# Kernel optimization log

Measured on AMD Instinct MI355X. Metric: run time of the kernel, lower is better.

## Reference

```python
import jax, jax.numpy as jnp
import numpy as np

IN_FEATURES = 1024
OUT_FEATURES = 1024
GRID_SIZE = 8
SPLINE_ORDER = 3
NUM_CTRL = GRID_SIZE + SPLINE_ORDER  # 11


def _make_grid():
    h = 2.0 / GRID_SIZE
    return jnp.linspace(-1.0 - SPLINE_ORDER * h, 1.0 + SPLINE_ORDER * h,
                        GRID_SIZE + 2 * SPLINE_ORDER + 1, dtype=jnp.float32)  # [15]


def b_splines(t, grid, order):
    # t: [B, F] (already tanh'd). Vectorized over all features at once —
    # the torch per-feature Python loop computes identical math per column.
    te = t[..., None]  # [B, F, 1]
    basis = ((te >= grid[:-1]) & (te < grid[1:])).astype(t.dtype)  # [B, F, G-1]
    for k in range(1, order + 1):
        left_den = grid[k:-1] - grid[:-k - 1]
        left_den = jnp.where(left_den == 0, jnp.ones_like(left_den), left_den)
        left = (te - grid[:-k - 1]) / left_den * basis[..., :-1]
        right_den = grid[k + 1:] - grid[1:-k]
        right_den = jnp.where(right_den == 0, jnp.ones_like(right_den), right_den)
        right = (grid[k + 1:] - te) / right_den * basis[..., 1:]
        basis = left + right
    return basis  # [B, F, NUM_CTRL]


def setup_inputs() -> dict:
    key = jax.random.key(0)
    kx, kc, kw = jax.random.split(key, 3)
    x = jax.random.normal(kx, (4096, IN_FEATURES), dtype=jnp.float32)
    coeffs = jax.random.normal(kc, (IN_FEATURES, OUT_FEATURES, NUM_CTRL), dtype=jnp.float32) * 0.05
    base_weight = jax.random.normal(kw, (IN_FEATURES, OUT_FEATURES), dtype=jnp.float32) * 0.05
    grid = _make_grid()
    return {"x": x, "coeffs": coeffs, "base_weight": base_weight, "grid": grid}


def reference(x, coeffs, base_weight, grid):
    bases = b_splines(jnp.tanh(x), grid, SPLINE_ORDER)          # [B, in, n]
    activation = jnp.einsum('bin,ion->bo', bases, coeffs)        # [B, out]
    residual = x @ base_weight                                   # [B, out]
    return activation + residual
```

## Files before the change

### kernel.cpp

```cpp
#include <hip/hip_runtime.h>
#include <hip/hip_bf16.h>

typedef __attribute__((ext_vector_type(8))) short bf16x8;
typedef __attribute__((ext_vector_type(4))) float f32x4;
typedef __attribute__((ext_vector_type(4))) unsigned short u16x4;
typedef __attribute__((ext_vector_type(8))) unsigned short u16x8;

#define M_DIM 4096
#define N_DIM 1024
#define IN_F  1024
#define K_DIM 12288
#define KS2   2
#define KPART2 (K_DIM / KS2)
#define BK 64
#define NT (KPART2 / BK)

__device__ __forceinline__ unsigned short f2b(float v) {
  __hip_bfloat16 h = __float2bfloat16(v);
  return *reinterpret_cast<unsigned short*>(&h);
}

__device__ __forceinline__ void spline12(float xv, float* w) {
  float t  = tanhf(xv);
  float tf = (t + 1.75f) * 4.0f;
  int j = (int)tf;
  j = j < 3 ? 3 : (j > 10 ? 10 : j);
  float u  = tf - (float)j;
  float um = 1.0f - u;
  float u2 = u * u;
  float w0 = um * um * um * (1.0f / 6.0f);
  float w1 = (0.5f * u - 1.0f) * u2 + (2.0f / 3.0f);
  float w2 = ((-0.5f * u + 0.5f) * u + 0.5f) * u + (1.0f / 6.0f);
  float w3 = u * u2 * (1.0f / 6.0f);
  int base = j - 3;
  #pragma unroll
  for (int s = 0; s < 11; ++s) {
    int r = s - base;
    w[s] = (r == 0) ? w0 : (r == 1) ? w1 : (r == 2) ? w2 : (r == 3) ? w3 : 0.0f;
  }
  w[11] = xv;
}

__global__ __launch_bounds__(256) void bases_kernel(const float* __restrict__ x,
                                                    unsigned short* __restrict__ A) {
  int e0 = blockIdx.x * 512 + threadIdx.x * 2;
  float2 xv = *(const float2*)(x + e0);
  float w0[12], w1[12];
  spline12(xv.x, w0);
  spline12(xv.y, w1);
  unsigned short h[24];
  #pragma unroll
  for (int s = 0; s < 12; ++s) { h[s] = f2b(w0[s]); h[12 + s] = f2b(w1[s]); }
  u16x8* dst = (u16x8*)(A + (size_t)e0 * 12);
  dst[0] = (u16x8){h[0],  h[1],  h[2],  h[3],  h[4],  h[5],  h[6],  h[7]};
  dst[1] = (u16x8){h[8],  h[9],  h[10], h[11], h[12], h[13], h[14], h[15]};
  dst[2] = (u16x8){h[16], h[17], h[18], h[19], h[20], h[21], h[22], h[23]};
}

__global__ __launch_bounds__(256) void repack_kernel(const float* __restrict__ coeffs,
                                                     const float* __restrict__ W,
                                                     unsigned short* __restrict__ Bt) {
  __shared__ float lc[64 * 176];
  __shared__ float lw[64 * 16];
  const int o0 = blockIdx.x * 16;
  const int i0 = blockIdx.y * 64;
  const int tid = threadIdx.x;
  #pragma unroll
  for (int it = 0; it < 11; ++it) {
    int v = it * 256 + tid;
    int i = v / 44, c = v - i * 44;
    f32x4 d = *(const f32x4*)(coeffs + ((size_t)(i0 + i) * 1024 + o0) * 11 + c * 4);
    *(f32x4*)(lc + i * 176 + c * 4) = d;
  }
  #pragma unroll
  for (int it = 0; it < 4; ++it) {
    int e = it * 256 + tid;
    int i = e >> 4, ol = e & 15;
    lw[e] = W[(size_t)(i0 + i) * 1024 + o0 + ol];
  }
  __syncthreads();
  #pragma unroll
  for (int it = 0; it < 6; ++it) {
    int v = it * 256 + tid;
    int ol = v / 96, c = v - ol * 96;
    unsigned short h[8];
    #pragma unroll
    for (int s = 0; s < 8; ++s) {
      int g = c * 8 + s;
      int i = g / 12, n = g - i * 12;
      float val = (n < 11) ? lc[i * 176 + ol * 11 + n] : lw[i * 16 + ol];
      h[s] = f2b(val);
    }
    *(u16x8*)(Bt + (size_t)(o0 + ol) * K_DIM + (size_t)i0 * 12 + c * 8) =
        (u16x8){h[0], h[1], h[2], h[3], h[4], h[5], h[6], h[7]};
  }
}

__device__ __forceinline__ void async16(const void* g, void* l) {
  __builtin_amdgcn_global_load_lds(
      (const __attribute__((address_space(1))) void*)g,
      (__attribute__((address_space(3))) void*)l, 16, 0, 0);
}

__global__ __launch_bounds__(512, 1) void gemm_kernel(const unsigned short* __restrict__ A,
                                                      const unsigned short* __restrict__ Bt,
                                                      float* __restrict__ out) {
  __shared__ __align__(16) unsigned short lds[73728];
  char* lp = (char*)lds;
  const int AS0 = 0, AS1 = 32768, AS2 = 65536;
  const int BS0 = 98304, BS1 = 98304 + 16384, BS2 = 98304 + 32768;

  const int tid  = threadIdx.x;
  const int lane = tid & 63;
  const int wid  = tid >> 6;
  const int wm   = wid >> 1;
  const int wn   = wid & 1;

  const int blk = blockIdx.x;
  const int bn  = blk & 7;
  const int r   = blk >> 3;
  const int bm  = r & 15;
  const int ks  = r >> 4;
  const size_t m0 = (size_t)bm * 256;
  const size_t n0 = (size_t)bn * 128;
  const size_t ksbyte = (size_t)ks * KPART2 * 2;

  const char* srcA[4]; int ldsA[4];
  #pragma unroll
  for (int q = 0; q < 4; ++q) {
    int g = q * 512 + tid;
    int rr = g >> 3, cp = g & 7;
    int cs = cp ^ (rr & 7);
    srcA[q] = (const char*)A + ((m0 + rr) * (size_t)K_DIM) * 2 + ksbyte + cs * 16;
    ldsA[q] = g * 16;
  }
  const char* srcB[2]; int ldsB[2];
  #pragma unroll
  for (int q = 0; q < 2; ++q) {
    int g = q * 512 + tid;
    int rr = g >> 3, cp = g & 7;
    int cs = cp ^ (rr & 7);
    srcB[q] = (const char*)Bt + ((n0 + rr) * (size_t)K_DIM) * 2 + ksbyte + cs * 16;
    ldsB[q] = g * 16;
  }

  auto stage = [&](int sa, int sb, int tile) {
    size_t kb = (size_t)tile * 128;
    #pragma unroll
    for (int q = 0; q < 4; ++q) async16(srcA[q] + kb, lp + sa + ldsA[q]);
    #pragma unroll
    for (int q = 0; q < 2; ++q) async16(srcB[q] + kb, lp + sb + ldsB[q]);
  };

  int offA[2][4], offB[2][4];
  #pragma unroll
  for (int kk = 0; kk < 2; ++kk) {
    #pragma unroll
    for (int m = 0; m < 4; ++m) {
      int row = wm * 64 + m * 16 + (lane & 15);
      int ck  = (kk * 4 + (lane >> 4)) ^ (row & 7);
      offA[kk][m] = row * 128 + ck * 16;
    }
    #pragma unroll
    for (int n = 0; n < 4; ++n) {
      int rowb = wn * 64 + n * 16 + (lane & 15);
      int ckb  = (kk * 4 + (lane >> 4)) ^ (rowb & 7);
      offB[kk][n] = rowb * 128 + ckb * 16;
    }
  }

  f32x4 acc[4][4];
  #pragma unroll
  for (int m = 0; m < 4; ++m)
    #pragma unroll
    for (int n = 0; n < 4; ++n) acc[m][n] = (f32x4){0.f, 0.f, 0.f, 0.f};

  stage(AS0, BS0, 0);
  stage(AS1, BS1, 1);
  stage(AS2, BS2, 2);

  int cA = AS0, nA = AS1, fA = AS2;
  int cB = BS0, nB = BS1, fB = BS2;

  for (int t = 0; t < NT; ++t) {
    if (t < NT - 2)       asm volatile("s_waitcnt vmcnt(12)" ::: "memory");
    else if (t == NT - 2) asm volatile("s_waitcnt vmcnt(6)"  ::: "memory");
    else                  asm volatile("s_waitcnt vmcnt(0)"  ::: "memory");
    __builtin_amdgcn_s_barrier();
    __builtin_amdgcn_sched_barrier(0);
    asm volatile("" ::: "memory");

    __builtin_amdgcn_s_setprio(1);
    #pragma unroll
    for (int kk = 0; kk < 2; ++kk) {
      bf16x8 a[4], b[4];
      #pragma unroll
      for (int m = 0; m < 4; ++m) a[m] = *(const bf16x8*)(lp + cA + offA[kk][m]);
      #pragma unroll
      for (int n = 0; n < 4; ++n) b[n] = *(const bf16x8*)(lp + cB + offB[kk][n]);
      #pragma unroll
      for (int m = 0; m < 4; ++m)
        #pragma unroll
        for (int n = 0; n < 4; ++n)
          acc[m][n] = __builtin_amdgcn_mfma_f32_16x16x32_bf16(a[m], b[n], acc[m][n], 0, 0, 0);
    }
    __builtin_amdgcn_s_setprio(0);

    asm volatile("" ::: "memory");
    __builtin_amdgcn_sched_barrier(0);
    __builtin_amdgcn_s_barrier();

    if (t + 3 < NT) stage(cA, cB, t + 3);

    int ta = cA; cA = nA; nA = fA; fA = ta;
    int tb = cB; cB = nB; nB = fB; fB = tb;
  }

  const int lr = (lane >> 4) * 4;
  const int lc = lane & 15;
  #pragma unroll
  for (int m = 0; m < 4; ++m)
    #pragma unroll
    for (int n = 0; n < 4; ++n)
      #pragma unroll
      for (int j = 0; j < 4; ++j)
        atomicAdd(&out[(m0 + wm * 64 + m * 16 + lr + j) * N_DIM + n0 + wn * 64 + n * 16 + lc],
                  acc[m][n][j]);
}

__global__ __launch_bounds__(256) void fallback_kernel(const float* __restrict__ x,
                                                       const float* __restrict__ coeffs,
                                                       const float* __restrict__ W,
                                                       float* __restrict__ out) {
  __shared__ float bas[16][64][12];
  const int o0 = blockIdx.x * 64;
  const int b0 = blockIdx.y * 16;
  const int tid = threadIdx.x;
  const int o = tid & 63, bg = tid >> 6;
  float acc[4] = {0.f, 0.f, 0.f, 0.f};
  for (int ic = 0; ic < 16; ++ic) {
    __syncthreads();
    #pragma unroll
    for (int p = 0; p < 4; ++p) {
      int pp = tid + p * 256;
      int bb = pp >> 6, il = pp & 63;
      float w[12];
      spline12(x[(size_t)(b0 + bb) * 1024 + ic * 64 + il], w);
      #pragma unroll
      for (int n = 0; n < 12; ++n) bas[bb][il][n] = w[n];
    }
    __syncthreads();
    for (int il = 0; il < 64; ++il) {
      int gi = ic * 64 + il;
      const float* cp = coeffs + ((size_t)gi * 1024 + o0 + o) * 11;
      float cf[12];
      #pragma unroll
      for (int n = 0; n < 11; ++n) cf[n] = cp[n];
      cf[11] = W[(size_t)gi * 1024 + o0 + o];
      #pragma unroll
      for (int bb = 0; bb < 4; ++bb) {
        float s = 0.f;
        #pragma unroll
        for (int n = 0; n < 12; ++n) s += bas[bg * 4 + bb][il][n] * cf[n];
        acc[bb] += s;
      }
    }
  }
  #pragma unroll
  for (int bb = 0; bb < 4; ++bb)
    out[(size_t)(b0 + bg * 4 + bb) * 1024 + o0 + o] = acc[bb];
}

extern "C" void kernel_launch(void* const* d_in, const int* in_sizes, int n_in,
                              void* d_out, int out_size, void* d_ws, size_t ws_size,
                              hipStream_t stream) {
  const float* x      = (const float*)d_in[0];
  const float* coeffs = (const float*)d_in[1];
  const float* W      = (const float*)d_in[2];
  float* out = (float*)d_out;

  const size_t needA = (size_t)M_DIM * K_DIM * 2;
  const size_t needB = (size_t)N_DIM * K_DIM * 2;

  if (ws_size >= needA + needB) {
    unsigned short* Abuf = (unsigned short*)d_ws;
    unsigned short* Btuf = (unsigned short*)((char*)d_ws + needA);
    hipMemsetAsync(out, 0, (size_t)out_size * sizeof(float), stream);
    bases_kernel<<<dim3(M_DIM * IN_F / 512), dim3(256), 0, stream>>>(x, Abuf);
    repack_kernel<<<dim3(64, 16), dim3(256), 0, stream>>>(coeffs, W, Btuf);
    gemm_kernel<<<dim3(16 * 8 * KS2), dim3(512), 0, stream>>>(Abuf, Btuf, out);
  } else {
    fallback_kernel<<<dim3(16, 256), dim3(256), 0, stream>>>(x, coeffs, W, out);
  }
}
```

Baseline: 276.7 us.

## Shrink GEMM tiles to 128x128 with double buffering and XCD-aware block mapping

The GEMM moves from 256x128 tiles with 512 threads and triple buffering to 128x128 tiles with 256 threads, double buffering and two blocks per CU. The grid grows to 512 blocks, and blocks are mapped so each XCD handles a contiguous set of M rows, which should help L2 reuse and occupancy. The bases kernel now stages its output through shared memory so global stores are coalesced, and repack LDS strides are padded to reduce bank conflicts. Smaller tiles reuse each loaded byte less, and two-stage buffering hides less latency than three.

New measurement: 236.9 us. 1.17x faster.

```diff
diff --git a/kernel.cpp b/kernel.cpp
--- a/kernel.cpp
+++ b/kernel.cpp
@@ -3,7 +3,6 @@
 
 typedef __attribute__((ext_vector_type(8))) short bf16x8;
 typedef __attribute__((ext_vector_type(4))) float f32x4;
-typedef __attribute__((ext_vector_type(4))) unsigned short u16x4;
 typedef __attribute__((ext_vector_type(8))) unsigned short u16x8;
 
 #define M_DIM 4096
@@ -11,9 +10,9 @@
 #define IN_F  1024
 #define K_DIM 12288
 #define KS2   2
-#define KPART2 (K_DIM / KS2)
+#define KPART (K_DIM / KS2)
 #define BK 64
-#define NT (KPART2 / BK)
+#define NT (KPART / BK)
 
 __device__ __forceinline__ unsigned short f2b(float v) {
   __hip_bfloat16 h = __float2bfloat16(v);
@@ -43,25 +42,27 @@
 
 __global__ __launch_bounds__(256) void bases_kernel(const float* __restrict__ x,
                                                     unsigned short* __restrict__ A) {
-  int e0 = blockIdx.x * 512 + threadIdx.x * 2;
+  __shared__ unsigned short sb[256 * 24];
+  const int tid = threadIdx.x;
+  int e0 = blockIdx.x * 512 + tid * 2;
   float2 xv = *(const float2*)(x + e0);
   float w0[12], w1[12];
   spline12(xv.x, w0);
   spline12(xv.y, w1);
-  unsigned short h[24];
-  #pragma unroll
-  for (int s = 0; s < 12; ++s) { h[s] = f2b(w0[s]); h[12 + s] = f2b(w1[s]); }
-  u16x8* dst = (u16x8*)(A + (size_t)e0 * 12);
-  dst[0] = (u16x8){h[0],  h[1],  h[2],  h[3],  h[4],  h[5],  h[6],  h[7]};
-  dst[1] = (u16x8){h[8],  h[9],  h[10], h[11], h[12], h[13], h[14], h[15]};
-  dst[2] = (u16x8){h[16], h[17], h[18], h[19], h[20], h[21], h[22], h[23]};
+  #pragma unroll
+  for (int s = 0; s < 12; ++s) { sb[tid * 24 + s] = f2b(w0[s]); sb[tid * 24 + 12 + s] = f2b(w1[s]); }
+  __syncthreads();
+  u16x8* dst = (u16x8*)(A + (size_t)blockIdx.x * 512 * 12);
+  const u16x8* src = (const u16x8*)sb;
+  #pragma unroll
+  for (int k = 0; k < 3; ++k) dst[tid + k * 256] = src[tid + k * 256];
 }
 
 __global__ __launch_bounds__(256) void repack_kernel(const float* __restrict__ coeffs,
                                                      const float* __restrict__ W,
                                                      unsigned short* __restrict__ Bt) {
-  __shared__ float lc[64 * 176];
-  __shared__ float lw[64 * 16];
+  __shared__ float lc[64 * 180];
+  __shared__ float lw[64 * 20];
   const int o0 = blockIdx.x * 16;
   const int i0 = blockIdx.y * 64;
   const int tid = threadIdx.x;
@@ -70,13 +71,13 @@
     int v = it * 256 + tid;
     int i = v / 44, c = v - i * 44;
     f32x4 d = *(const f32x4*)(coeffs + ((size_t)(i0 + i) * 1024 + o0) * 11 + c * 4);
-    *(f32x4*)(lc + i * 176 + c * 4) = d;
+    *(f32x4*)(lc + i * 180 + c * 4) = d;
   }
   #pragma unroll
   for (int it = 0; it < 4; ++it) {
     int e = it * 256 + tid;
     int i = e >> 4, ol = e & 15;
-    lw[e] = W[(size_t)(i0 + i) * 1024 + o0 + ol];
+    lw[i * 20 + ol] = W[(size_t)(i0 + i) * 1024 + o0 + ol];
   }
   __syncthreads();
   #pragma unroll
@@ -88,7 +89,7 @@
     for (int s = 0; s < 8; ++s) {
       int g = c * 8 + s;
       int i = g / 12, n = g - i * 12;
-      float val = (n < 11) ? lc[i * 176 + ol * 11 + n] : lw[i * 16 + ol];
+      float val = (n < 11) ? lc[i * 180 + ol * 11 + n] : lw[i * 20 + ol];
       h[s] = f2b(val);
     }
     *(u16x8*)(Bt + (size_t)(o0 + ol) * K_DIM + (size_t)i0 * 12 + c * 8) =
@@ -102,54 +103,47 @@
       (__attribute__((address_space(3))) void*)l, 16, 0, 0);
 }
 
-__global__ __launch_bounds__(512, 1) void gemm_kernel(const unsigned short* __restrict__ A,
+__global__ __launch_bounds__(256, 2) void gemm_kernel(const unsigned short* __restrict__ A,
                                                       const unsigned short* __restrict__ Bt,
                                                       float* __restrict__ out) {
-  __shared__ __align__(16) unsigned short lds[73728];
+  __shared__ __align__(16) unsigned short lds[32768];
   char* lp = (char*)lds;
-  const int AS0 = 0, AS1 = 32768, AS2 = 65536;
-  const int BS0 = 98304, BS1 = 98304 + 16384, BS2 = 98304 + 32768;
+  const int AS[2] = {0, 16384};
+  const int BS[2] = {32768, 49152};
 
   const int tid  = threadIdx.x;
   const int lane = tid & 63;
   const int wid  = tid >> 6;
-  const int wm   = wid >> 1;
-  const int wn   = wid & 1;
+  const int wm   = wid >> 1, wn = wid & 1;
 
   const int blk = blockIdx.x;
-  const int bn  = blk & 7;
-  const int r   = blk >> 3;
-  const int bm  = r & 15;
-  const int ks  = r >> 4;
-  const size_t m0 = (size_t)bm * 256;
+  const int xcd = blk & 7;
+  const int idx = blk >> 3;
+  const int bn  = idx & 7;
+  const int p   = idx >> 3;
+  const int bm  = xcd * 4 + (p & 3);
+  const int ks  = p >> 2;
+  const size_t m0 = (size_t)bm * 128;
   const size_t n0 = (size_t)bn * 128;
-  const size_t ksbyte = (size_t)ks * KPART2 * 2;
-
-  const char* srcA[4]; int ldsA[4];
+  const size_t ksbyte = (size_t)ks * KPART * 2;
+
+  const char* srcA[4]; const char* srcB[4]; int ldso[4];
   #pragma unroll
   for (int q = 0; q < 4; ++q) {
-    int g = q * 512 + tid;
+    int g  = q * 256 + tid;
     int rr = g >> 3, cp = g & 7;
     int cs = cp ^ (rr & 7);
-    srcA[q] = (const char*)A + ((m0 + rr) * (size_t)K_DIM) * 2 + ksbyte + cs * 16;
-    ldsA[q] = g * 16;
-  }
-  const char* srcB[2]; int ldsB[2];
-  #pragma unroll
-  for (int q = 0; q < 2; ++q) {
-    int g = q * 512 + tid;
-    int rr = g >> 3, cp = g & 7;
-    int cs = cp ^ (rr & 7);
+    srcA[q] = (const char*)A  + ((m0 + rr) * (size_t)K_DIM) * 2 + ksbyte + cs * 16;
     srcB[q] = (const char*)Bt + ((n0 + rr) * (size_t)K_DIM) * 2 + ksbyte + cs * 16;
-    ldsB[q] = g * 16;
-  }
-
-  auto stage = [&](int sa, int sb, int tile) {
+    ldso[q] = g * 16;
+  }
+
+  auto stage = [&](int slot, int tile) {
     size_t kb = (size_t)tile * 128;
     #pragma unroll
-    for (int q = 0; q < 4; ++q) async16(srcA[q] + kb, lp + sa + ldsA[q]);
-    #pragma unroll
-    for (int q = 0; q < 2; ++q) async16(srcB[q] + kb, lp + sb + ldsB[q]);
+    for (int q = 0; q < 4; ++q) async16(srcA[q] + kb, lp + AS[slot] + ldso[q]);
+    #pragma unroll
+    for (int q = 0; q < 4; ++q) async16(srcB[q] + kb, lp + BS[slot] + ldso[q]);
   };
 
   int offA[2][4], offB[2][4];
@@ -160,12 +154,9 @@
       int row = wm * 64 + m * 16 + (lane & 15);
       int ck  = (kk * 4 + (lane >> 4)) ^ (row & 7);
       offA[kk][m] = row * 128 + ck * 16;
-    }
-    #pragma unroll
-    for (int n = 0; n < 4; ++n) {
-      int rowb = wn * 64 + n * 16 + (lane & 15);
+      int rowb = wn * 64 + m * 16 + (lane & 15);
       int ckb  = (kk * 4 + (lane >> 4)) ^ (rowb & 7);
-      offB[kk][n] = rowb * 128 + ckb * 16;
+      offB[kk][m] = rowb * 128 + ckb * 16;
     }
   }
 
@@ -175,17 +166,13 @@
     #pragma unroll
     for (int n = 0; n < 4; ++n) acc[m][n] = (f32x4){0.f, 0.f, 0.f, 0.f};
 
-  stage(AS0, BS0, 0);
-  stage(AS1, BS1, 1);
-  stage(AS2, BS2, 2);
-
-  int cA = AS0, nA = AS1, fA = AS2;
-  int cB = BS0, nB = BS1, fB = BS2;
+  stage(0, 0);
+  stage(1, 1);
 
   for (int t = 0; t < NT; ++t) {
-    if (t < NT - 2)       asm volatile("s_waitcnt vmcnt(12)" ::: "memory");
-    else if (t == NT - 2) asm volatile("s_waitcnt vmcnt(6)"  ::: "memory");
-    else                  asm volatile("s_waitcnt vmcnt(0)"  ::: "memory");
+    const int cur = t & 1;
+    if (t < NT - 1) asm volatile("s_waitcnt vmcnt(8)" ::: "memory");
+    else            asm volatile("s_waitcnt vmcnt(0)" ::: "memory");
     __builtin_amdgcn_s_barrier();
     __builtin_amdgcn_sched_barrier(0);
     asm volatile("" ::: "memory");
@@ -195,9 +182,9 @@
     for (int kk = 0; kk < 2; ++kk) {
       bf16x8 a[4], b[4];
       #pragma unroll
-      for (int m = 0; m < 4; ++m) a[m] = *(const bf16x8*)(lp + cA + offA[kk][m]);
-      #pragma unroll
-      for (int n = 0; n < 4; ++n) b[n] = *(const bf16x8*)(lp + cB + offB[kk][n]);
+      for (int m = 0; m < 4; ++m) a[m] = *(const bf16x8*)(lp + AS[cur] + offA[kk][m]);
+      #pragma unroll
+      for (int n = 0; n < 4; ++n) b[n] = *(const bf16x8*)(lp + BS[cur] + offB[kk][n]);
       #pragma unroll
       for (int m = 0; m < 4; ++m)
         #pragma unroll
@@ -210,10 +197,7 @@
     __builtin_amdgcn_sched_barrier(0);
     __builtin_amdgcn_s_barrier();
 
-    if (t + 3 < NT) stage(cA, cB, t + 3);
-
-    int ta = cA; cA = nA; nA = fA; fA = ta;
-    int tb = cB; cB = nB; nB = fB; fB = tb;
+    if (t + 2 < NT) stage(cur, t + 2);
   }
 
   const int lr = (lane >> 4) * 4;
@@ -288,7 +272,7 @@
     hipMemsetAsync(out, 0, (size_t)out_size * sizeof(float), stream);
     bases_kernel<<<dim3(M_DIM * IN_F / 512), dim3(256), 0, stream>>>(x, Abuf);
     repack_kernel<<<dim3(64, 16), dim3(256), 0, stream>>>(coeffs, W, Btuf);
-    gemm_kernel<<<dim3(16 * 8 * KS2), dim3(512), 0, stream>>>(Abuf, Btuf, out);
+    gemm_kernel<<<dim3(32 * 8 * KS2 / 2 * 2), dim3(256), 0, stream>>>(Abuf, Btuf, out);
   } else {
     fallback_kernel<<<dim3(16, 256), dim3(256), 0, stream>>>(x, coeffs, W, out);
   }
```
